# Performance work log

Measured on AMD Instinct MI355X. Metric: run time of the kernel, lower is better.

The kernel has to match this reference:

```python
import jax, jax.numpy as jnp
import numpy as np

INNER_DIM = 1024

def setup_inputs() -> dict:
    key = jax.random.key(0)
    ks = jax.random.split(key, 6)
    b, n, d = 4, 4096, 1024
    s = 0.02
    return {
        "x": jax.random.normal(ks[0], (b, n, d), jnp.float32),
        "y": jax.random.normal(ks[1], (b, n, d), jnp.float32),
        "Wq": jax.random.normal(ks[2], (INNER_DIM, d), jnp.float32) * s,
        "Wk": jax.random.normal(ks[3], (INNER_DIM, d), jnp.float32) * s,
        "Wv": jax.random.normal(ks[4], (INNER_DIM, d), jnp.float32) * s,
        "Wo": jax.random.normal(ks[5], (d, INNER_DIM), jnp.float32) * s,
        "bo": jnp.zeros((d,), jnp.float32),
    }

def reference(x, y, Wq, Wk, Wv, Wo, bo):
    # torch Linear: out = inp @ W.T ; weights stored [out_dim, in_dim]
    q = jnp.einsum('bnd,ed->bne', y, Wq)  # queries come from y
    k = jnp.einsum('bnd,ed->bne', x, Wk)
    v = jnp.einsum('bnd,ed->bne', x, Wv)
    dk = 1.0 / jnp.sqrt(jnp.asarray(INNER_DIM, q.dtype))  # full inner_dim, not per-head
    alpha = jnp.einsum('bie,bje->bij', q, k) * dk  # [b, n, n] full score matrix
    alpha = jax.nn.softmax(alpha, axis=-1)
    # NOTE: original masked_fill is a no-op (result discarded), so no causal mask.
    ctx = jnp.einsum('bij,bje->bie', alpha, v)
    return jnp.einsum('bie,de->bid', ctx, Wo) + bo
```

## Files before the change

kernel.cpp:

```cpp
#include <hip/hip_runtime.h>
#include <stdint.h>

typedef __attribute__((ext_vector_type(8))) short s16x8;
typedef __attribute__((ext_vector_type(4))) float f32x4;

__device__ __forceinline__ unsigned short f2bf(float f) {
    union { float f; uint32_t u; } c; c.f = f;
    uint32_t u = c.u + 0x7FFFu + ((c.u >> 16) & 1u);
    return (unsigned short)(u >> 16);
}

__device__ __forceinline__ float bf2f(unsigned int u16) {
    union { uint32_t u; float f; } c; c.u = u16 << 16;
    return c.f;
}

__device__ __forceinline__ void load_lds16(const unsigned short* g, unsigned short* l) {
    __builtin_amdgcn_global_load_lds(
        (const __attribute__((address_space(1))) char*)(uintptr_t)g,
        (__attribute__((address_space(3))) char*)(uint32_t)(uintptr_t)l,
        16, 0, 0);
}

__device__ __forceinline__ void gemm256_core(
    const unsigned short* __restrict__ Ap, long lda,
    const unsigned short* __restrict__ Bp, long ldb,
    int nt, unsigned short* As, unsigned short* Bs, f32x4 (*acc)[4])
{
    (void)ldb;
    const int tid  = threadIdx.x;
    const int wv   = tid >> 6;
    const int lane = tid & 63;
    const int cl   = lane & 15;
    const int qd   = lane >> 4;
    const int wm   = wv >> 2;
    const int wn   = wv & 3;

    long src[2][2];
    int  dstL[2][2];
#pragma unroll
    for (int h = 0; h < 2; ++h)
#pragma unroll
        for (int c = 0; c < 2; ++c) {
            const int q0    = (wv << 7) + (c << 6);
            const int phys0 = q0 + (q0 & 512) + (h << 9);
            const int phys  = phys0 + lane;
            const int g     = phys >> 3;
            const long koff = (long)(((lane & 7) ^ (g & 7)) << 3);
            src[h][c]  = (long)g * lda + koff;
            dstL[h][c] = phys0 << 3;
        }

    const int k0off = (((qd    ) ^ (cl & 7)) << 3) + cl * 64;
    const int k1off = (((4 + qd) ^ (cl & 7)) << 3) + cl * 64;
    const int aB = wm << 3;
    const int bB = wn << 2;

#define STAGE_A(buf, kb, h) do {                                             \
        load_lds16(Ap + (kb) + src[h][0], As + ((buf) << 14) + dstL[h][0]);  \
        load_lds16(Ap + (kb) + src[h][1], As + ((buf) << 14) + dstL[h][1]);  \
    } while (0)
#define STAGE_B(buf, kb, h) do {                                             \
        load_lds16(Bp + (kb) + src[h][0], Bs + ((buf) << 14) + dstL[h][0]);  \
        load_lds16(Bp + (kb) + src[h][1], Bs + ((buf) << 14) + dstL[h][1]);  \
    } while (0)
#define VMW(n) asm volatile("s_waitcnt vmcnt(" #n ")" ::: "memory")
#define VMLG(n) asm volatile("s_waitcnt vmcnt(" #n ") lgkmcnt(0)" ::: "memory")
#define BAR()  asm volatile("s_barrier" ::: "memory")
#define READ_AF(DST, AB, S0) do {                                            \
        _Pragma("unroll")                                                    \
        for (int i_ = 0; i_ < 2; ++i_) {                                     \
            const int s_ = aB + (S0) + i_;                                   \
            DST[i_][0] = *(const s16x8*)&As[((AB) << 14) + s_ * 1024 + k0off];\
            DST[i_][1] = *(const s16x8*)&As[((AB) << 14) + s_ * 1024 + k1off];\
        }                                                                    \
    } while (0)
#define READ_BF(BB) do {                                                     \
        _Pragma("unroll")                                                    \
        for (int j_ = 0; j_ < 4; ++j_) {                                     \
            const int s_ = bB + j_;                                          \
            bfr[j_][0] = *(const s16x8*)&Bs[((BB) << 14) + s_ * 1024 + k0off];\
            bfr[j_][1] = *(const s16x8*)&Bs[((BB) << 14) + s_ * 1024 + k1off];\
        }                                                                    \
    } while (0)
#define MFMA16(B0, AF) do {                                                  \
        __builtin_amdgcn_s_setprio(1);                                       \
        _Pragma("unroll")                                                    \
        for (int i_ = 0; i_ < 2; ++i_)                                       \
            _Pragma("unroll")                                                \
            for (int j_ = 0; j_ < 4; ++j_) {                                 \
                acc[(B0) + i_][j_] =                                         \
                    __builtin_amdgcn_mfma_f32_16x16x32_bf16(                 \
                        AF[i_][0], bfr[j_][0], acc[(B0) + i_][j_], 0, 0, 0); \
                acc[(B0) + i_][j_] =                                         \
                    __builtin_amdgcn_mfma_f32_16x16x32_bf16(                 \
                        AF[i_][1], bfr[j_][1], acc[(B0) + i_][j_], 0, 0, 0); \
            }                                                                \
        __builtin_amdgcn_s_setprio(0);                                       \
    } while (0)

    STAGE_B(0, 0, 0); STAGE_B(0, 0, 1); STAGE_A(0, 0, 0); STAGE_A(0, 0, 1);
    STAGE_B(1, 64, 0); STAGE_B(1, 64, 1); STAGE_A(1, 64, 0);
    VMW(8);
    BAR();

    s16x8 bfr[4][2], afX[2][2], afY[2][2];
    READ_AF(afX, 0, 0);

    const int ni = nt >> 1;
#pragma unroll 1
    for (int it = 0; it < ni; ++it) {
        const bool more = (it + 1) < ni;
        const long kb_o  = ((long)(2 * it + 1)) << 6;
        const long kb_e2 = ((long)(2 * it + 2)) << 6;
        const long kb_o2 = ((long)(2 * it + 3)) << 6;

        READ_BF(0);
        READ_AF(afY, 0, 2);
        STAGE_A(1, kb_o, 1);
        VMLG(8);
        BAR();
        MFMA16(0, afX);
        READ_AF(afX, 0, 4);
        if (more) STAGE_B(0, kb_e2, 0);
        BAR();
        MFMA16(2, afY);
        READ_AF(afY, 0, 6);
        if (more) { STAGE_B(0, kb_e2, 1); VMW(6); } else VMW(2);
        BAR();
        MFMA16(4, afX);
        READ_AF(afX, 1, 0);
        if (more) STAGE_A(0, kb_e2, 0);
        BAR();
        MFMA16(6, afY);
        READ_BF(1);
        READ_AF(afY, 1, 2);
        if (more) { STAGE_A(0, kb_e2, 1); VMLG(8); } else VMLG(0);
        BAR();
        MFMA16(0, afX);
        READ_AF(afX, 1, 4);
        if (more) STAGE_B(1, kb_o2, 0);
        BAR();
        MFMA16(2, afY);
        READ_AF(afY, 1, 6);
        if (more) { STAGE_B(1, kb_o2, 1); VMW(6); }
        BAR();
        MFMA16(4, afX);
        if (more) { READ_AF(afX, 0, 0); STAGE_A(1, kb_o2, 0); }
        BAR();
        MFMA16(6, afY);
    }
#undef STAGE_A
#undef STAGE_B
#undef VMW
#undef VMLG
#undef BAR
#undef READ_AF
#undef READ_BF
#undef MFMA16
}

template <bool OUT_BF16, bool HAS_BIAS, bool EXP_OUT>
__global__ __launch_bounds__(512, 2)
void gemm256(const unsigned short* __restrict__ A, long lda, long sA,
             const unsigned short* __restrict__ B, long ldb, long sB,
             void* __restrict__ C, long ldc, long sC,
             const float* __restrict__ bias, int K, float scale)
{
    __shared__ __align__(16) unsigned short As[2 * 16384];
    __shared__ __align__(16) unsigned short Bs[2 * 16384];

    const unsigned gx = gridDim.x, gy = gridDim.y;
    const unsigned lin = blockIdx.x + gx * blockIdx.y;
    unsigned bxs, bys;
    if ((gy & 7u) == 0u) {
        const unsigned g = lin & 7u, j = lin >> 3;
        bxs = j & (gx - 1u);
        bys = g * (gy >> 3) + j / gx;
    } else { bxs = blockIdx.x; bys = blockIdx.y; }

    const unsigned short* Ap = A + (long)blockIdx.z * sA + (long)bys * 256 * lda;
    const unsigned short* Bp = B + (long)blockIdx.z * sB + (long)bxs * 256 * ldb;

    f32x4 acc[8][4];
#pragma unroll
    for (int i = 0; i < 8; ++i)
#pragma unroll
        for (int j = 0; j < 4; ++j)
            acc[i][j] = f32x4{0.f, 0.f, 0.f, 0.f};

    gemm256_core(Ap, lda, Bp, ldb, K >> 6, As, Bs, acc);

    const int wv = threadIdx.x >> 6;
    const int wm = wv >> 2, wn = wv & 3;
    const int cl = threadIdx.x & 15, qd = (threadIdx.x & 63) >> 4;
    const long row0 = (long)bys * 256 + wm * 128;
    const long col0 = (long)bxs * 256 + wn * 64;
    const long zC   = (long)blockIdx.z * sC;
#pragma unroll
    for (int j = 0; j < 4; ++j) {
        const long c = col0 + j * 16 + cl;
        float badd = 0.f;
        if constexpr (HAS_BIAS) badd = bias[c];
#pragma unroll
        for (int i = 0; i < 8; ++i) {
            const long rb = row0 + i * 16 + qd * 4;
#pragma unroll
            for (int r = 0; r < 4; ++r) {
                float v = acc[i][j][r] * scale + badd;
                if constexpr (EXP_OUT) v = __expf(v);
                const long idx = zC + (rb + r) * ldc + c;
                if constexpr (OUT_BF16) ((unsigned short*)C)[idx] = f2bf(v);
                else                    ((float*)C)[idx] = v;
            }
        }
    }
}

__global__ __launch_bounds__(512, 2)
void gemm256_sc4(const unsigned short* __restrict__ Q, long lda, long sAB,
                 const unsigned short* __restrict__ Kp,
                 unsigned short* __restrict__ o0, unsigned short* __restrict__ o1,
                 unsigned short* __restrict__ o2, unsigned short* __restrict__ o3,
                 long ldc, float* __restrict__ rsum, int K, float scale)
{
    __shared__ __align__(16) unsigned short As[2 * 16384];
    __shared__ __align__(16) unsigned short Bs[2 * 16384];

    const unsigned gx = gridDim.x, gy = gridDim.y;
    const unsigned lin = blockIdx.x + gx * blockIdx.y;
    unsigned bxs, bys;
    if ((gy & 7u) == 0u) {
        const unsigned g = lin & 7u, j = lin >> 3;
        bxs = j & (gx - 1u);
        bys = g * (gy >> 3) + j / gx;
    } else { bxs = blockIdx.x; bys = blockIdx.y; }

    const int z = blockIdx.z;
    unsigned short* Co = (z == 0) ? o0 : (z == 1) ? o1 : (z == 2) ? o2 : o3;

    const unsigned short* Ap = Q  + (long)z * sAB + (long)bys * 256 * lda;
    const unsigned short* Bp = Kp + (long)z * sAB + (long)bxs * 256 * lda;

    f32x4 acc[8][4];
#pragma unroll
    for (int i = 0; i < 8; ++i)
#pragma unroll
        for (int j = 0; j < 4; ++j)
            acc[i][j] = f32x4{0.f, 0.f, 0.f, 0.f};

    gemm256_core(Ap, lda, Bp, lda, K >> 6, As, Bs, acc);

    const int wv = threadIdx.x >> 6;
    const int wm = wv >> 2, wn = wv & 3;
    const int cl = threadIdx.x & 15, qd = (threadIdx.x & 63) >> 4;
    const long row0 = (long)bys * 256 + wm * 128;
    const long col0 = (long)bxs * 256 + wn * 64;
    float* rs = rsum + (long)z * 4096;
#pragma unroll
    for (int i = 0; i < 8; ++i) {
        const long rb = row0 + i * 16 + qd * 4;
#pragma unroll
        for (int r = 0; r < 4; ++r) {
            float s = 0.f;
#pragma unroll
            for (int j = 0; j < 4; ++j) {
                const float v = __expf(acc[i][j][r] * scale);
                const unsigned short h = f2bf(v);
                Co[(rb + r) * ldc + col0 + j * 16 + cl] = h;
                s += bf2f(h);
            }
            s += __shfl_xor(s, 1);
            s += __shfl_xor(s, 2);
            s += __shfl_xor(s, 4);
            s += __shfl_xor(s, 8);
            if (cl == 0) atomicAdd(&rs[rb + r], s);
        }
    }
}

__global__ __launch_bounds__(512, 2)
void gemm256_pv4(const unsigned short* __restrict__ p0,
                 const unsigned short* __restrict__ p1,
                 const unsigned short* __restrict__ p2,
                 const unsigned short* __restrict__ p3,
                 const unsigned short* __restrict__ Bv, long ldb, long sB,
                 unsigned short* __restrict__ C, long ldc, long sC,
                 const float* __restrict__ rowdiv, int K, long lda)
{
    __shared__ __align__(16) unsigned short As[2 * 16384];
    __shared__ __align__(16) unsigned short Bs[2 * 16384];

    const unsigned gx = gridDim.x, gy = gridDim.y;
    const unsigned lin = blockIdx.x + gx * blockIdx.y;
    unsigned bxs, bys;
    if ((gy & 7u) == 0u) {
        const unsigned g = lin & 7u, j = lin >> 3;
        bxs = j & (gx - 1u);
        bys = g * (gy >> 3) + j / gx;
    } else { bxs = blockIdx.x; bys = blockIdx.y; }

    const int z = blockIdx.z;
    const unsigned short* A = (z == 0) ? p0 : (z == 1) ? p1 : (z == 2) ? p2 : p3;

    const unsigned short* Ap = A + (long)bys * 256 * lda;
    const unsigned short* Bp = Bv + (long)z * sB + (long)bxs * 256 * ldb;

    f32x4 acc[8][4];
#pragma unroll
    for (int i = 0; i < 8; ++i)
#pragma unroll
        for (int j = 0; j < 4; ++j)
            acc[i][j] = f32x4{0.f, 0.f, 0.f, 0.f};

    gemm256_core(Ap, lda, Bp, ldb, K >> 6, As, Bs, acc);

    const int wv = threadIdx.x >> 6;
    const int wm = wv >> 2, wn = wv & 3;
    const int cl = threadIdx.x & 15, qd = (threadIdx.x & 63) >> 4;
    const long row0 = (long)bys * 256 + wm * 128;
    const long col0 = (long)bxs * 256 + wn * 64;
    const long zC   = (long)z * sC;
    const float* rd = rowdiv + (long)z * 4096;
#pragma unroll
    for (int i = 0; i < 8; ++i) {
        const long rb = row0 + i * 16 + qd * 4;
        float rinv[4];
#pragma unroll
        for (int r = 0; r < 4; ++r) rinv[r] = 1.f / rd[rb + r];
#pragma unroll
        for (int j = 0; j < 4; ++j) {
            const long c = col0 + j * 16 + cl;
#pragma unroll
            for (int r = 0; r < 4; ++r)
                C[zC + (rb + r) * ldc + c] = f2bf(acc[i][j][r] * rinv[r]);
        }
    }
}

__global__ __launch_bounds__(256)
void cast2_bf16(const float* __restrict__ s0, unsigned short* __restrict__ d0,
                const float* __restrict__ s1, unsigned short* __restrict__ d1)
{
    const float*    in  = blockIdx.y ? s1 : s0;
    unsigned short* out = blockIdx.y ? d1 : d0;
    const long i = ((long)blockIdx.x * 256 + threadIdx.x) * 4;
    const float4 v = *(const float4*)(in + i);
    ushort4 o;
    o.x = f2bf(v.x); o.y = f2bf(v.y); o.z = f2bf(v.z); o.w = f2bf(v.w);
    *(ushort4*)(out + i) = o;
}

__global__ __launch_bounds__(256)
void cast4_bf16(const float* __restrict__ s0, unsigned short* __restrict__ d0,
                const float* __restrict__ s1, unsigned short* __restrict__ d1,
                const float* __restrict__ s2, unsigned short* __restrict__ d2,
                const float* __restrict__ s3, unsigned short* __restrict__ d3)
{
    const float* in; unsigned short* out;
    switch (blockIdx.y) {
        case 0: in = s0; out = d0; break;
        case 1: in = s1; out = d1; break;
        case 2: in = s2; out = d2; break;
        default: in = s3; out = d3; break;
    }
    const long i = ((long)blockIdx.x * 256 + threadIdx.x) * 4;
    const float4 v = *(const float4*)(in + i);
    ushort4 o;
    o.x = f2bf(v.x); o.y = f2bf(v.y); o.z = f2bf(v.z); o.w = f2bf(v.w);
    *(ushort4*)(out + i) = o;
}

extern "C" void kernel_launch(void* const* d_in, const int* in_sizes, int n_in,
                              void* d_out, int out_size, void* d_ws, size_t ws_size,
                              hipStream_t stream)
{
    (void)in_sizes; (void)n_in; (void)out_size;
    const float* x  = (const float*)d_in[0];
    const float* y  = (const float*)d_in[1];
    const float* Wq = (const float*)d_in[2];
    const float* Wk = (const float*)d_in[3];
    const float* Wv = (const float*)d_in[4];
    const float* Wo = (const float*)d_in[5];
    const float* bo = (const float*)d_in[6];
    float* out = (float*)d_out;

    const long N = 4096, D = 1024;
    const long NB = N * D;
    const size_t MiB = 1ull << 20;
    const float dk = 0.03125f;
    char* w = (char*)d_ws;

    if (ws_size >= 200 * MiB) {
        unsigned short* Xb  = (unsigned short*)(w);
        unsigned short* Yb  = (unsigned short*)(w + 32 * MiB);
        unsigned short* Qb  = (unsigned short*)(w + 64 * MiB);
        unsigned short* Kb  = (unsigned short*)(w + 96 * MiB);
        unsigned short* VT  = (unsigned short*)(w + 128 * MiB);
        unsigned short* Wqb = (unsigned short*)(w + 192 * MiB);
        unsigned short* Wkb = (unsigned short*)(w + 194 * MiB);
        unsigned short* Wvb = (unsigned short*)(w + 196 * MiB);
        unsigned short* Wob = (unsigned short*)(w + 198 * MiB);
        unsigned short* P0  = (unsigned short*)(w);
        unsigned short* P1  = (unsigned short*)(w + 32 * MiB);
        unsigned short* P2  = (unsigned short*)(w + 160 * MiB);
        unsigned short* P3  = (unsigned short*)d_out;
        unsigned short* Cx  = (unsigned short*)(w + 64 * MiB);
        float*          rsm = (float*)(w + 192 * MiB);

        cast2_bf16<<<dim3(16384, 2), dim3(256), 0, stream>>>(x, Xb, y, Yb);
        cast4_bf16<<<dim3(1024, 4),  dim3(256), 0, stream>>>(
            Wq, Wqb, Wk, Wkb, Wv, Wvb, Wo, Wob);

        gemm256<true, false, false><<<dim3(4, 64, 2), dim3(512), 0, stream>>>(
            Yb, D, (long)(Xb - Yb), Wqb, D, (long)(Wkb - Wqb),
            Qb, D, (long)(Kb - Qb), nullptr, (int)D, 1.f);
        gemm256<true, false, false><<<dim3(16, 4, 4), dim3(512), 0, stream>>>(
            Wvb, D, 0, Xb, D, NB, VT, N, NB, nullptr, (int)D, 1.f);
        hipMemsetAsync(rsm, 0, 4 * 16384 * sizeof(float), stream);

        gemm256_sc4<<<dim3(16, 16, 4), dim3(512), 0, stream>>>(
            Qb, D, NB, Kb, P0, P1, P2, P3, N, rsm, (int)D, dk);

        gemm256_pv4<<<dim3(4, 16, 4), dim3(512), 0, stream>>>(
            P0, P1, P2, P3, VT, N, NB, Cx, D, NB, rsm, (int)N, N);
        gemm256<false, true, false><<<dim3(4, 64, 1), dim3(512), 0, stream>>>(
            Cx, D, 0, Wob, D, 0, out, D, 0, bo, (int)D, 1.f);
    } else if (ws_size >= 104 * MiB) {
        unsigned short* Wqb = (unsigned short*)(w);
        unsigned short* Wkb = (unsigned short*)(w + 2 * MiB);
        unsigned short* Wvb = (unsigned short*)(w + 4 * MiB);
        unsigned short* Wob = (unsigned short*)(w + 6 * MiB);
        unsigned short* xb  = (unsigned short*)(w + 8 * MiB);
        unsigned short* yb  = (unsigned short*)(w + 16 * MiB);
        unsigned short* Qb  = (unsigned short*)(w + 24 * MiB);
        unsigned short* Kb  = (unsigned short*)(w + 32 * MiB);
        unsigned short* VTb = (unsigned short*)(w + 40 * MiB);
        unsigned short* Cxb = (unsigned short*)(w + 48 * MiB);
        unsigned short* Pb  = (unsigned short*)(w + 56 * MiB);
        float*          rsm = (float*)(w + 88 * MiB);

        cast4_bf16<<<dim3(1024, 4), dim3(256), 0, stream>>>(
            Wq, Wqb, Wk, Wkb, Wv, Wvb, Wo, Wob);

        for (int b = 0; b < 4; ++b) {
            cast2_bf16<<<dim3(4096, 2), dim3(256), 0, stream>>>(
                x + b * NB, xb, y + b * NB, yb);
            gemm256<true, false, false><<<dim3(4, 16, 1), dim3(512), 0, stream>>>(
                yb, D, 0, Wqb, D, 0, Qb, D, 0, nullptr, (int)D, 1.f);
            gemm256<true, false, false><<<dim3(4, 16, 1), dim3(512), 0, stream>>>(
                xb, D, 0, Wkb, D, 0, Kb, D, 0, nullptr, (int)D, 1.f);
            gemm256<true, false, false><<<dim3(16, 4, 1), dim3(512), 0, stream>>>(
                Wvb, D, 0, xb, D, 0, VTb, N, 0, nullptr, (int)D, 1.f);
            hipMemsetAsync(rsm, 0, 16384 * sizeof(float), stream);
            gemm256_sc4<<<dim3(16, 16, 1), dim3(512), 0, stream>>>(
                Qb, D, 0, Kb, Pb, Pb, Pb, Pb, N, rsm, (int)D, dk);
            gemm256_pv4<<<dim3(4, 16, 1), dim3(512), 0, stream>>>(
                Pb, Pb, Pb, Pb, VTb, N, 0, Cxb, D, 0, rsm, (int)N, N);
            gemm256<false, true, false><<<dim3(4, 16, 1), dim3(512), 0, stream>>>(
                Cxb, D, 0, Wob, D, 0, out + b * NB, D, 0, bo, (int)D, 1.f);
        }
    }
}
```

Before: 604.0 us.

## Double-buffer B fragments and move barriers after MFMA blocks in GEMM main loop

Adds a second register set for B fragments (bfrX/bfrY), so B reads for the next half-tile are issued before the current MFMAs instead of stalling at the start of each half. Each barrier now comes after its MFMA block rather than before it, and the explicit lgkmcnt(0) waits are removed. The aim is to overlap LDS reads and global→LDS staging with matrix math. It costs more VGPRs under the 512x2 launch bounds, which risks spills, and the reordered waits and barriers risk LDS read/write hazards.

```diff
diff --git a/kernel.cpp b/kernel.cpp
--- a/kernel.cpp
+++ b/kernel.cpp
@@ -65,7 +65,6 @@
         load_lds16(Bp + (kb) + src[h][1], Bs + ((buf) << 14) + dstL[h][1]);  \
     } while (0)
 #define VMW(n) asm volatile("s_waitcnt vmcnt(" #n ")" ::: "memory")
-#define VMLG(n) asm volatile("s_waitcnt vmcnt(" #n ") lgkmcnt(0)" ::: "memory")
 #define BAR()  asm volatile("s_barrier" ::: "memory")
 #define READ_AF(DST, AB, S0) do {                                            \
         _Pragma("unroll")                                                    \
@@ -75,15 +74,15 @@
             DST[i_][1] = *(const s16x8*)&As[((AB) << 14) + s_ * 1024 + k1off];\
         }                                                                    \
     } while (0)
-#define READ_BF(BB) do {                                                     \
+#define READ_BF(DST, BB) do {                                                \
         _Pragma("unroll")                                                    \
         for (int j_ = 0; j_ < 4; ++j_) {                                     \
             const int s_ = bB + j_;                                          \
-            bfr[j_][0] = *(const s16x8*)&Bs[((BB) << 14) + s_ * 1024 + k0off];\
-            bfr[j_][1] = *(const s16x8*)&Bs[((BB) << 14) + s_ * 1024 + k1off];\
+            DST[j_][0] = *(const s16x8*)&Bs[((BB) << 14) + s_ * 1024 + k0off];\
+            DST[j_][1] = *(const s16x8*)&Bs[((BB) << 14) + s_ * 1024 + k1off];\
         }                                                                    \
     } while (0)
-#define MFMA16(B0, AF) do {                                                  \
+#define MFMA16(B0, AF, BF) do {                                              \
         __builtin_amdgcn_s_setprio(1);                                       \
         _Pragma("unroll")                                                    \
         for (int i_ = 0; i_ < 2; ++i_)                                       \
@@ -91,20 +90,21 @@
             for (int j_ = 0; j_ < 4; ++j_) {                                 \
                 acc[(B0) + i_][j_] =                                         \
                     __builtin_amdgcn_mfma_f32_16x16x32_bf16(                 \
-                        AF[i_][0], bfr[j_][0], acc[(B0) + i_][j_], 0, 0, 0); \
+                        AF[i_][0], BF[j_][0], acc[(B0) + i_][j_], 0, 0, 0);  \
                 acc[(B0) + i_][j_] =                                         \
                     __builtin_amdgcn_mfma_f32_16x16x32_bf16(                 \
-                        AF[i_][1], bfr[j_][1], acc[(B0) + i_][j_], 0, 0, 0); \
+                        AF[i_][1], BF[j_][1], acc[(B0) + i_][j_], 0, 0, 0);  \
             }                                                                \
         __builtin_amdgcn_s_setprio(0);                                       \
     } while (0)
 
     STAGE_B(0, 0, 0); STAGE_B(0, 0, 1); STAGE_A(0, 0, 0); STAGE_A(0, 0, 1);
     STAGE_B(1, 64, 0); STAGE_B(1, 64, 1); STAGE_A(1, 64, 0);
-    VMW(8);
+    VMW(6);
     BAR();
 
-    s16x8 bfr[4][2], afX[2][2], afY[2][2];
+    s16x8 bfrX[4][2], bfrY[4][2], afX[2][2], afY[2][2];
+    READ_BF(bfrX, 0);
     READ_AF(afX, 0, 0);
 
     const int ni = nt >> 1;
@@ -115,45 +115,46 @@
         const long kb_e2 = ((long)(2 * it + 2)) << 6;
         const long kb_o2 = ((long)(2 * it + 3)) << 6;
 
-        READ_BF(0);
+        BAR();
         READ_AF(afY, 0, 2);
         STAGE_A(1, kb_o, 1);
-        VMLG(8);
-        BAR();
-        MFMA16(0, afX);
+        MFMA16(0, afX, bfrX);
+        VMW(8);
+        BAR();
         READ_AF(afX, 0, 4);
         if (more) STAGE_B(0, kb_e2, 0);
-        BAR();
-        MFMA16(2, afY);
+        MFMA16(2, afY, bfrX);
+        BAR();
         READ_AF(afY, 0, 6);
-        if (more) { STAGE_B(0, kb_e2, 1); VMW(6); } else VMW(2);
-        BAR();
-        MFMA16(4, afX);
+        if (more) STAGE_B(0, kb_e2, 1);
+        MFMA16(4, afX, bfrX);
+        if (more) VMW(6); else VMW(2);
+        BAR();
         READ_AF(afX, 1, 0);
+        READ_BF(bfrY, 1);
         if (more) STAGE_A(0, kb_e2, 0);
-        BAR();
-        MFMA16(6, afY);
-        READ_BF(1);
+        MFMA16(6, afY, bfrX);
+        BAR();
         READ_AF(afY, 1, 2);
-        if (more) { STAGE_A(0, kb_e2, 1); VMLG(8); } else VMLG(0);
-        BAR();
-        MFMA16(0, afX);
+        if (more) STAGE_A(0, kb_e2, 1);
+        MFMA16(0, afX, bfrY);
+        if (more) VMW(8); else VMW(0);
+        BAR();
         READ_AF(afX, 1, 4);
         if (more) STAGE_B(1, kb_o2, 0);
-        BAR();
-        MFMA16(2, afY);
+        MFMA16(2, afY, bfrY);
+        BAR();
         READ_AF(afY, 1, 6);
-        if (more) { STAGE_B(1, kb_o2, 1); VMW(6); }
-        BAR();
-        MFMA16(4, afX);
-        if (more) { READ_AF(afX, 0, 0); STAGE_A(1, kb_o2, 0); }
-        BAR();
-        MFMA16(6, afY);
+        if (more) STAGE_B(1, kb_o2, 1);
+        MFMA16(4, afX, bfrY);
+        if (more) VMW(6);
+        BAR();
+        if (more) { READ_AF(afX, 0, 0); READ_BF(bfrX, 0); STAGE_A(1, kb_o2, 0); }
+        MFMA16(6, afY, bfrY);
     }
 #undef STAGE_A
 #undef STAGE_B
 #undef VMW
-#undef VMLG
 #undef BAR
 #undef READ_AF
 #undef READ_BF
```

New measurement: 1.004 ms. +66.2%, slower.
